# Performance work log

Measured on AMD Instinct MI355X. Metric: run time of the kernel, lower is better.

Reference implementation:

```python
import jax, jax.numpy as jnp
import numpy as np

S, B, E = 512, 512, 768

def setup_inputs() -> dict:
    key = jax.random.key(0)
    k1, k2, k3 = jax.random.split(key, 3)
    inputs = jax.random.normal(k1, (S, B, E), dtype=jnp.float32)
    rotation_params = jax.random.normal(k2, (E, E), dtype=jnp.float32)
    entangle_params = jax.random.normal(k3, (E, E), dtype=jnp.float32)
    return {"inputs": inputs, "rotation_params": rotation_params, "entangle_params": entangle_params}

def reference(inputs, rotation_params, entangle_params):
    seq_len, batch, embed_dim = inputs.shape
    # Q/K projections: (S,B,E) @ (E,E) -> (S,B,E)
    q = jnp.einsum('sbe,ef->sbf', inputs, rotation_params.reshape(embed_dim, -1))
    k = jnp.einsum('sbe,ef->sbf', inputs, entangle_params.reshape(embed_dim, -1))
    v = inputs
    # Faithful to the torch code: matmul batches over seq_len, so attention
    # mixes across the BATCH axis -> scores shape (S, B, B).
    scale = 1.0 / jnp.sqrt(jnp.float32(embed_dim))
    scores = jax.nn.softmax(jnp.einsum('sbe,sce->sbc', q, k) * scale, axis=-1)
    return jnp.einsum('sbc,sce->sbe', scores, v)
```

## Files before the change

kernel.cpp:

```cpp
#include <hip/hip_runtime.h>
#include <hip/hip_bf16.h>
#include <math.h>

typedef unsigned short ushort_t;
typedef __attribute__((ext_vector_type(8))) short bf16x8;
typedef __attribute__((ext_vector_type(4))) float f32x4;

#define SCALE 0.03608439182435161f

__device__ __forceinline__ ushort_t f2bf(float f) {
  unsigned u = __float_as_uint(f);
  return (ushort_t)((u + 0x7FFFu + ((u >> 16) & 1u)) >> 16);
}
__device__ __forceinline__ float bf2f(ushort_t h) {
  return __uint_as_float(((unsigned)h) << 16);
}

__device__ __forceinline__ void split4(float4 v, ushort_t* hh, ushort_t* ll) {
  __hip_bfloat162 h01 = __float22bfloat162_rn(make_float2(v.x, v.y));
  __hip_bfloat162 h23 = __float22bfloat162_rn(make_float2(v.z, v.w));
  unsigned u01 = *(unsigned*)&h01, u23 = *(unsigned*)&h23;
  float l0 = v.x - __uint_as_float((u01 & 0xFFFFu) << 16);
  float l1 = v.y - __uint_as_float(u01 & 0xFFFF0000u);
  float l2 = v.z - __uint_as_float((u23 & 0xFFFFu) << 16);
  float l3 = v.w - __uint_as_float(u23 & 0xFFFF0000u);
  __hip_bfloat162 g01 = __float22bfloat162_rn(make_float2(l0, l1));
  __hip_bfloat162 g23 = __float22bfloat162_rn(make_float2(l2, l3));
  *(unsigned*)&hh[0] = u01; *(unsigned*)&hh[2] = u23;
  *(unsigned*)&ll[0] = *(unsigned*)&g01; *(unsigned*)&ll[2] = *(unsigned*)&g23;
}

struct MMP {
  const float* Af;  long aLd;
  const float* Bf;
  const ushort_t* Bhi; const ushort_t* Blo; long bLd;
  ushort_t* Chi; ushort_t* Clo; long cLd;
  int zMode;
  int K;
};

template <int BM>
__global__ __launch_bounds__(256) void mm(MMP P)
{
  __shared__ ushort_t lds[16384];
  ushort_t* Ah = lds;
  ushort_t* Al = lds + 4096;
  ushort_t* Bh = lds + 8192;
  ushort_t* Bl = lds + 12288;

  const int tid = threadIdx.x;
  int bx = blockIdx.x, by = blockIdx.y;
  {
    int nwg = gridDim.x * gridDim.y;
    if ((nwg & 7) == 0) {
      int id = by * gridDim.x + bx;
      int q = nwg >> 3;
      int wid = (id & 7) * q + (id >> 3);
      bx = wid % gridDim.x;
      by = wid / gridDim.x;
    }
  }
  const int m0 = by * 128, n0 = bx * 128;

  const int lane = tid & 63;
  const int wave = tid >> 6;
  const int wm = (wave >> 1) * 64, wn = (wave & 1) * 64;
  const int lr = lane & 15, g = lane >> 4;

  f32x4 acc[4][4];
  #pragma unroll
  for (int i = 0; i < 4; ++i)
    #pragma unroll
    for (int j = 0; j < 4; ++j) {
      f32x4 zv = {0.f, 0.f, 0.f, 0.f};
      acc[i][j] = zv;
    }

  for (int k0 = 0; k0 < P.K; k0 += 32) {
    #pragma unroll
    for (int rep = 0; rep < 4; ++rep) {
      int idx = tid + rep * 256;
      int row = idx >> 3, q = idx & 7;
      float4 v = *(const float4*)(P.Af + (long)(m0 + row) * P.aLd + k0 + q * 4);
      int off = row * 32 + (((q >> 1) ^ ((row >> 1) & 3)) << 3) + ((q & 1) << 2);
      ushort_t hh[4], ll[4];
      split4(v, hh, ll);
      *(uint2*)(Ah + off) = *(uint2*)hh;
      *(uint2*)(Al + off) = *(uint2*)ll;
    }
    if constexpr (BM == 0) {
      #pragma unroll
      for (int rep = 0; rep < 4; ++rep) {
        int idx = tid + rep * 256;
        int row = idx >> 3, q = idx & 7;
        float4 v = *(const float4*)(P.Bf + (long)(n0 + row) * P.bLd + k0 + q * 4);
        int off = row * 32 + (((q >> 1) ^ ((row >> 1) & 3)) << 3) + ((q & 1) << 2);
        ushort_t hh[4], ll[4];
        split4(v, hh, ll);
        *(uint2*)(Bh + off) = *(uint2*)hh;
        *(uint2*)(Bl + off) = *(uint2*)ll;
      }
    } else {
      #pragma unroll
      for (int rep = 0; rep < 2; ++rep) {
        int idx = tid + rep * 256;
        int row = idx >> 2, h8 = idx & 3;
        int off = row * 32 + ((h8 ^ ((row >> 1) & 3)) << 3);
        long gsrc = (long)(n0 + row) * P.bLd + k0 + h8 * 8;
        *(uint4*)(Bh + off) = *(const uint4*)(P.Bhi + gsrc);
        *(uint4*)(Bl + off) = *(const uint4*)(P.Blo + gsrc);
      }
    }
    __syncthreads();

    bf16x8 ar[4], br[4];
    #pragma unroll
    for (int i = 0; i < 4; ++i) {
      int row = wm + i * 16 + lr;
      ar[i] = *(const bf16x8*)(Ah + row * 32 + ((g ^ ((row >> 1) & 3)) << 3));
    }
    #pragma unroll
    for (int j = 0; j < 4; ++j) {
      int row = wn + j * 16 + lr;
      br[j] = *(const bf16x8*)(Bh + row * 32 + ((g ^ ((row >> 1) & 3)) << 3));
    }
    #pragma unroll
    for (int i = 0; i < 4; ++i)
      #pragma unroll
      for (int j = 0; j < 4; ++j)
        acc[i][j] = __builtin_amdgcn_mfma_f32_16x16x32_bf16(ar[i], br[j], acc[i][j], 0, 0, 0);
    #pragma unroll
    for (int j = 0; j < 4; ++j) {
      int row = wn + j * 16 + lr;
      bf16x8 blv = *(const bf16x8*)(Bl + row * 32 + ((g ^ ((row >> 1) & 3)) << 3));
      #pragma unroll
      for (int i = 0; i < 4; ++i)
        acc[i][j] = __builtin_amdgcn_mfma_f32_16x16x32_bf16(ar[i], blv, acc[i][j], 0, 0, 0);
    }
    #pragma unroll
    for (int i = 0; i < 4; ++i) {
      int row = wm + i * 16 + lr;
      bf16x8 alv = *(const bf16x8*)(Al + row * 32 + ((g ^ ((row >> 1) & 3)) << 3));
      #pragma unroll
      for (int j = 0; j < 4; ++j)
        acc[i][j] = __builtin_amdgcn_mfma_f32_16x16x32_bf16(alv, br[j], acc[i][j], 0, 0, 0);
    }
    __syncthreads();
  }

  #pragma unroll
  for (int i = 0; i < 4; ++i) {
    #pragma unroll
    for (int j = 0; j < 4; ++j) {
      int colG = n0 + wn + j * 16 + lr;
      #pragma unroll
      for (int r = 0; r < 4; ++r) {
        int rowG = m0 + wm + i * 16 + g * 4 + r;
        float v = acc[i][j][r];
        ushort_t hi = f2bf(v);
        ushort_t lo = f2bf(v - bf2f(hi));
        long off;
        if (P.zMode) off = (long)(rowG >> 9) * 786432 + (long)(rowG & 511) * 1536 + colG;
        else         off = (long)rowG * P.cLd + colG;
        P.Chi[off] = hi;
        P.Clo[off] = lo;
      }
    }
  }
}

__global__ __launch_bounds__(512) void fsc5(ushort_t* __restrict__ slots,
                                            const float* __restrict__ X)
{
  __shared__ ushort_t lds[36864];
  ushort_t* Ah = lds;
  ushort_t* Al = lds + 2048;
  ushort_t* Bh = lds + 4096;
  ushort_t* Bl = lds + 20480;
  float* redf = (float*)lds;
  float* reds = (float*)lds + 768;

  const int id = blockIdx.x;
  const int c = id & 7, r = id >> 3;
  const int tile = r & 7;
  const int s = c + ((r >> 3) << 3);
  const int m0 = tile * 64;

  ushort_t* Az = slots + (long)s * 786432;
  const float* Xf = X + (long)s * 393216;

  const int tid = threadIdx.x;
  const int lane = tid & 63;
  const int wave = tid >> 6;
  const int wn = wave * 64;
  const int lr = lane & 15, g = lane >> 4;

  f32x4 acc[4][4];
  #pragma unroll
  for (int i = 0; i < 4; ++i)
    #pragma unroll
    for (int j = 0; j < 4; ++j) {
      f32x4 zv = {0.f, 0.f, 0.f, 0.f};
      acc[i][j] = zv;
    }

  for (int k0 = 0; k0 < 768; k0 += 32) {
    {
      int e = tid & 255;
      int row = e >> 2, h8 = e & 3;
      int off = row * 32 + ((h8 ^ ((row >> 1) & 3)) << 3);
      long src = (long)(m0 + row) * 1536 + k0 + h8 * 8;
      if (tid < 256) *(uint4*)(Ah + off) = *(const uint4*)(Az + src);
      else           *(uint4*)(Al + off) = *(const uint4*)(Az + src + 768);
    }
    #pragma unroll
    for (int rep = 0; rep < 8; ++rep) {
      int idx = tid + rep * 512;
      int row = idx >> 3, q = idx & 7;
      float4 v = *(const float4*)(Xf + (long)row * 768 + k0 + q * 4);
      int off = row * 32 + (((q >> 1) ^ ((row >> 1) & 3)) << 3) + ((q & 1) << 2);
      ushort_t hh[4], ll[4];
      split4(v, hh, ll);
      *(uint2*)(Bh + off) = *(uint2*)hh;
      *(uint2*)(Bl + off) = *(uint2*)ll;
    }
    __syncthreads();

    bf16x8 arh[4], arl[4];
    #pragma unroll
    for (int i = 0; i < 4; ++i) {
      int row = i * 16 + lr;
      int off = row * 32 + ((g ^ ((row >> 1) & 3)) << 3);
      arh[i] = *(const bf16x8*)(Ah + off);
      arl[i] = *(const bf16x8*)(Al + off);
    }
    #pragma unroll
    for (int j = 0; j < 4; ++j) {
      int row = wn + j * 16 + lr;
      int off = row * 32 + ((g ^ ((row >> 1) & 3)) << 3);
      bf16x8 bh = *(const bf16x8*)(Bh + off);
      bf16x8 bl = *(const bf16x8*)(Bl + off);
      #pragma unroll
      for (int i = 0; i < 4; ++i) {
        acc[i][j] = __builtin_amdgcn_mfma_f32_16x16x32_bf16(arh[i], bh, acc[i][j], 0, 0, 0);
        acc[i][j] = __builtin_amdgcn_mfma_f32_16x16x32_bf16(arh[i], bl, acc[i][j], 0, 0, 0);
        acc[i][j] = __builtin_amdgcn_mfma_f32_16x16x32_bf16(arl[i], bh, acc[i][j], 0, 0, 0);
      }
    }
    __syncthreads();
  }

  float mr[4][4];
  #pragma unroll
  for (int i = 0; i < 4; ++i)
    #pragma unroll
    for (int rg = 0; rg < 4; ++rg) {
      float mx = -3.0e38f;
      #pragma unroll
      for (int j = 0; j < 4; ++j) {
        acc[i][j][rg] *= SCALE;
        mx = fmaxf(mx, acc[i][j][rg]);
      }
      #pragma unroll
      for (int off = 8; off >= 1; off >>= 1) mx = fmaxf(mx, __shfl_xor(mx, off, 64));
      if (lr == 0) redf[(i * 16 + g * 4 + rg) * 12 + wave] = mx;
    }
  __syncthreads();
  #pragma unroll
  for (int i = 0; i < 4; ++i)
    #pragma unroll
    for (int rg = 0; rg < 4; ++rg) {
      int row = i * 16 + g * 4 + rg;
      float4 a = *(const float4*)&redf[row * 12];
      float4 b = *(const float4*)&redf[row * 12 + 4];
      mr[i][rg] = fmaxf(fmaxf(fmaxf(a.x, a.y), fmaxf(a.z, a.w)),
                        fmaxf(fmaxf(b.x, b.y), fmaxf(b.z, b.w)));
    }
  #pragma unroll
  for (int i = 0; i < 4; ++i)
    #pragma unroll
    for (int rg = 0; rg < 4; ++rg) {
      float sm = 0.f;
      #pragma unroll
      for (int j = 0; j < 4; ++j) {
        float e = __expf(acc[i][j][rg] - mr[i][rg]);
        acc[i][j][rg] = e;
        sm += e;
      }
      #pragma unroll
      for (int off = 8; off >= 1; off >>= 1) sm += __shfl_xor(sm, off, 64);
      if (lr == 0) reds[(i * 16 + g * 4 + rg) * 12 + wave] = sm;
    }
  __syncthreads();
  #pragma unroll
  for (int i = 0; i < 4; ++i)
    #pragma unroll
    for (int rg = 0; rg < 4; ++rg) {
      int row = i * 16 + g * 4 + rg;
      float4 a = *(const float4*)&reds[row * 12];
      float4 b = *(const float4*)&reds[row * 12 + 4];
      float inv = 1.0f / (a.x + a.y + a.z + a.w + b.x + b.y + b.z + b.w);
      #pragma unroll
      for (int j = 0; j < 4; ++j)
        Az[(long)(m0 + row) * 1536 + wn + j * 16 + lr] = f2bf(acc[i][j][rg] * inv);
    }
}

__global__ __launch_bounds__(768) void pv(float* __restrict__ outp,
                                          const float* __restrict__ X)
{
  __shared__ ushort_t Pa[32768];

  const int id = blockIdx.x;
  const int c = id & 7, r = id >> 3;
  const int tile = r & 7;
  const int s = c + ((r >> 3) << 3);
  const int m0 = tile * 64;

  const ushort_t* Ps = (const ushort_t*)outp + (long)s * 786432;
  const float* Xf = X + (long)s * 393216;

  const int tid = threadIdx.x;
  const int lane = tid & 63;
  const int wave = tid >> 6;
  const int wn = wave * 64;
  const int lr = lane & 15, g = lane >> 4;

  for (int idx = tid; idx < 4096; idx += 768) {
    int row = idx >> 6, h8 = idx & 63;
    int off = row * 512 + ((h8 ^ (row & 7)) << 3);
    *(uint4*)(Pa + off) = *(const uint4*)(Ps + (long)(m0 + row) * 1536 + h8 * 8);
  }
  __syncthreads();

  f32x4 acc[4][4];
  #pragma unroll
  for (int i = 0; i < 4; ++i)
    #pragma unroll
    for (int j = 0; j < 4; ++j) {
      f32x4 zv = {0.f, 0.f, 0.f, 0.f};
      acc[i][j] = zv;
    }

  for (int kk = 0; kk < 16; ++kk) {
    const int k0 = kk * 32;
    bf16x8 ar[4];
    #pragma unroll
    for (int i = 0; i < 4; ++i) {
      int row = i * 16 + lr;
      ar[i] = *(const bf16x8*)(Pa + row * 512 + (((kk * 4 + g) ^ (row & 7)) << 3));
    }
    #pragma unroll
    for (int j = 0; j < 4; ++j) {
      int col = wn + j * 16 + lr;
      float xv[8];
      #pragma unroll
      for (int i = 0; i < 8; ++i)
        xv[i] = Xf[(long)(k0 + g * 8 + i) * 768 + col];
      unsigned w[4];
      #pragma unroll
      for (int p = 0; p < 4; ++p) {
        __hip_bfloat162 hb = __float22bfloat162_rn(make_float2(xv[2 * p], xv[2 * p + 1]));
        w[p] = *(unsigned*)&hb;
      }
      bf16x8 bv = *(bf16x8*)w;
      #pragma unroll
      for (int i = 0; i < 4; ++i)
        acc[i][j] = __builtin_amdgcn_mfma_f32_16x16x32_bf16(ar[i], bv, acc[i][j], 0, 0, 0);
    }
  }

  float* Co = outp + (long)s * 393216;
  #pragma unroll
  for (int i = 0; i < 4; ++i)
    #pragma unroll
    for (int j = 0; j < 4; ++j) {
      int colG = wn + j * 16 + lr;
      #pragma unroll
      for (int rg = 0; rg < 4; ++rg) {
        int rowG = m0 + i * 16 + g * 4 + rg;
        Co[(long)rowG * 768 + colG] = acc[i][j][rg];
      }
    }
}

extern "C" void kernel_launch(void* const* d_in, const int* in_sizes, int n_in,
                              void* d_out, int out_size, void* d_ws, size_t ws_size,
                              hipStream_t stream) {
  const float* X = (const float*)d_in[0];
  const float* R = (const float*)d_in[1];
  const float* W = (const float*)d_in[2];

  ushort_t* Hhi = (ushort_t*)d_ws;
  ushort_t* Hlo = Hhi + 768 * 768;

  {
    MMP p{};
    p.Af = W; p.aLd = 768;
    p.Bf = R; p.bLd = 768;
    p.Chi = Hhi; p.Clo = Hlo; p.cLd = 768; p.zMode = 0;
    p.K = 768;
    mm<0><<<dim3(6, 6), 256, 0, stream>>>(p);
  }
  {
    MMP p{};
    p.Af = X; p.aLd = 768;
    p.Bhi = Hhi; p.Blo = Hlo; p.bLd = 768;
    p.Chi = (ushort_t*)d_out;
    p.Clo = (ushort_t*)d_out + 768;
    p.zMode = 1;
    p.K = 768;
    mm<1><<<dim3(6, 2048), 256, 0, stream>>>(p);
  }
  fsc5<<<dim3(4096), 512, 0, stream>>>((ushort_t*)d_out, X);
  pv<<<dim3(4096), 768, 0, stream>>>((float*)d_out, X);
}
```

Baseline: 3.074 ms.

## Double-buffer LDS tiles in score kernel with register prefetch of next K slice

The score kernel now keeps two LDS buffers. It prefetches the next K slice of A and X into registers while MFMAs run on the current buffer, then writes the prefetch into the other buffer, so each step needs one barrier instead of two. The MFMA loop is also reordered into three independent passes over all 16 accumulators so that dependent MFMAs are spaced further apart. The cost is twice the LDS footprint (144KB) and many more live registers, and a launch_bounds hint of 2 blocks per CU that the LDS size may not allow.

After: 3.113 ms. Within noise of the previous version (+1.2%).

```diff
diff --git a/kernel.cpp b/kernel.cpp
--- a/kernel.cpp
+++ b/kernel.cpp
@@ -169,14 +169,10 @@
   }
 }
 
-__global__ __launch_bounds__(512) void fsc5(ushort_t* __restrict__ slots,
-                                            const float* __restrict__ X)
+__global__ __launch_bounds__(512, 2) void fsc6(ushort_t* __restrict__ slots,
+                                               const float* __restrict__ X)
 {
-  __shared__ ushort_t lds[36864];
-  ushort_t* Ah = lds;
-  ushort_t* Al = lds + 2048;
-  ushort_t* Bh = lds + 4096;
-  ushort_t* Bl = lds + 20480;
+  __shared__ ushort_t lds[73728];
   float* redf = (float*)lds;
   float* reds = (float*)lds + 768;
 
@@ -195,6 +191,12 @@
   const int wn = wave * 64;
   const int lr = lane & 15, g = lane >> 4;
 
+  const int ae = tid & 255;
+  const int arow = ae >> 2, ah8 = ae & 3;
+  const int aoff = arow * 32 + ((ah8 ^ ((arow >> 1) & 3)) << 3);
+  const long asrc = (long)(m0 + arow) * 1536 + ah8 * 8 + (tid < 256 ? 0 : 768);
+  const int adst = aoff + (tid < 256 ? 0 : 2048);
+
   f32x4 acc[4][4];
   #pragma unroll
   for (int i = 0; i < 4; ++i)
@@ -204,49 +206,90 @@
       acc[i][j] = zv;
     }
 
-  for (int k0 = 0; k0 < 768; k0 += 32) {
-    {
-      int e = tid & 255;
-      int row = e >> 2, h8 = e & 3;
-      int off = row * 32 + ((h8 ^ ((row >> 1) & 3)) << 3);
-      long src = (long)(m0 + row) * 1536 + k0 + h8 * 8;
-      if (tid < 256) *(uint4*)(Ah + off) = *(const uint4*)(Az + src);
-      else           *(uint4*)(Al + off) = *(const uint4*)(Az + src + 768);
-    }
-    #pragma unroll
-    for (int rep = 0; rep < 8; ++rep) {
-      int idx = tid + rep * 512;
-      int row = idx >> 3, q = idx & 7;
-      float4 v = *(const float4*)(Xf + (long)row * 768 + k0 + q * 4);
-      int off = row * 32 + (((q >> 1) ^ ((row >> 1) & 3)) << 3) + ((q & 1) << 2);
-      ushort_t hh[4], ll[4];
-      split4(v, hh, ll);
-      *(uint2*)(Bh + off) = *(uint2*)hh;
-      *(uint2*)(Bl + off) = *(uint2*)ll;
-    }
-    __syncthreads();
-
-    bf16x8 arh[4], arl[4];
+  float4 bv0, bv1, bv2, bv3, bv4, bv5, bv6, bv7;
+  uint4 av;
+
+#define FSC_LOAD(K0)                                                         \
+  do {                                                                       \
+    av = *(const uint4*)(Az + asrc + (K0));                                  \
+    const float* xb = Xf + (K0);                                             \
+    bv0 = *(const float4*)(xb + (long)((tid + 0 * 512) >> 3) * 768 + ((tid + 0 * 512) & 7) * 4); \
+    bv1 = *(const float4*)(xb + (long)((tid + 1 * 512) >> 3) * 768 + ((tid + 1 * 512) & 7) * 4); \
+    bv2 = *(const float4*)(xb + (long)((tid + 2 * 512) >> 3) * 768 + ((tid + 2 * 512) & 7) * 4); \
+    bv3 = *(const float4*)(xb + (long)((tid + 3 * 512) >> 3) * 768 + ((tid + 3 * 512) & 7) * 4); \
+    bv4 = *(const float4*)(xb + (long)((tid + 4 * 512) >> 3) * 768 + ((tid + 4 * 512) & 7) * 4); \
+    bv5 = *(const float4*)(xb + (long)((tid + 5 * 512) >> 3) * 768 + ((tid + 5 * 512) & 7) * 4); \
+    bv6 = *(const float4*)(xb + (long)((tid + 6 * 512) >> 3) * 768 + ((tid + 6 * 512) & 7) * 4); \
+    bv7 = *(const float4*)(xb + (long)((tid + 7 * 512) >> 3) * 768 + ((tid + 7 * 512) & 7) * 4); \
+  } while (0)
+
+#define FSC_WR1(BH, BL, BV, REP)                                             \
+  do {                                                                       \
+    int idx = tid + (REP) * 512;                                             \
+    int row = idx >> 3, q = idx & 7;                                         \
+    int off = row * 32 + (((q >> 1) ^ ((row >> 1) & 3)) << 3) + ((q & 1) << 2); \
+    ushort_t hh[4], ll[4];                                                   \
+    split4(BV, hh, ll);                                                      \
+    *(uint2*)((BH) + off) = *(uint2*)hh;                                     \
+    *(uint2*)((BL) + off) = *(uint2*)ll;                                     \
+  } while (0)
+
+#define FSC_WRITE(B)                                                         \
+  do {                                                                       \
+    ushort_t* Ab = lds + (B) * 4096;                                         \
+    ushort_t* Bhw = lds + 8192 + (B) * 32768;                                \
+    ushort_t* Blw = Bhw + 16384;                                             \
+    *(uint4*)(Ab + adst) = av;                                               \
+    FSC_WR1(Bhw, Blw, bv0, 0); FSC_WR1(Bhw, Blw, bv1, 1);                    \
+    FSC_WR1(Bhw, Blw, bv2, 2); FSC_WR1(Bhw, Blw, bv3, 3);                    \
+    FSC_WR1(Bhw, Blw, bv4, 4); FSC_WR1(Bhw, Blw, bv5, 5);                    \
+    FSC_WR1(Bhw, Blw, bv6, 6); FSC_WR1(Bhw, Blw, bv7, 7);                    \
+  } while (0)
+
+  FSC_LOAD(0);
+  FSC_WRITE(0);
+  __syncthreads();
+
+  for (int t = 0; t < 24; ++t) {
+    const int cb = t & 1;
+    if (t < 23) FSC_LOAD((t + 1) * 32);
+
+    const ushort_t* Ab = lds + cb * 4096;
+    const ushort_t* Bh = lds + 8192 + cb * 32768;
+    const ushort_t* Bl = Bh + 16384;
+
+    bf16x8 arh[4], arl[4], bh[4], bl[4];
     #pragma unroll
     for (int i = 0; i < 4; ++i) {
       int row = i * 16 + lr;
       int off = row * 32 + ((g ^ ((row >> 1) & 3)) << 3);
-      arh[i] = *(const bf16x8*)(Ah + off);
-      arl[i] = *(const bf16x8*)(Al + off);
+      arh[i] = *(const bf16x8*)(Ab + off);
+      arl[i] = *(const bf16x8*)(Ab + 2048 + off);
     }
     #pragma unroll
     for (int j = 0; j < 4; ++j) {
       int row = wn + j * 16 + lr;
       int off = row * 32 + ((g ^ ((row >> 1) & 3)) << 3);
-      bf16x8 bh = *(const bf16x8*)(Bh + off);
-      bf16x8 bl = *(const bf16x8*)(Bl + off);
-      #pragma unroll
-      for (int i = 0; i < 4; ++i) {
-        acc[i][j] = __builtin_amdgcn_mfma_f32_16x16x32_bf16(arh[i], bh, acc[i][j], 0, 0, 0);
-        acc[i][j] = __builtin_amdgcn_mfma_f32_16x16x32_bf16(arh[i], bl, acc[i][j], 0, 0, 0);
-        acc[i][j] = __builtin_amdgcn_mfma_f32_16x16x32_bf16(arl[i], bh, acc[i][j], 0, 0, 0);
-      }
-    }
+      bh[j] = *(const bf16x8*)(Bh + off);
+      bl[j] = *(const bf16x8*)(Bl + off);
+    }
+    #pragma unroll
+    for (int i = 0; i < 4; ++i)
+      #pragma unroll
+      for (int j = 0; j < 4; ++j)
+        acc[i][j] = __builtin_amdgcn_mfma_f32_16x16x32_bf16(arh[i], bh[j], acc[i][j], 0, 0, 0);
+    #pragma unroll
+    for (int i = 0; i < 4; ++i)
+      #pragma unroll
+      for (int j = 0; j < 4; ++j)
+        acc[i][j] = __builtin_amdgcn_mfma_f32_16x16x32_bf16(arh[i], bl[j], acc[i][j], 0, 0, 0);
+    #pragma unroll
+    for (int i = 0; i < 4; ++i)
+      #pragma unroll
+      for (int j = 0; j < 4; ++j)
+        acc[i][j] = __builtin_amdgcn_mfma_f32_16x16x32_bf16(arl[i], bh[j], acc[i][j], 0, 0, 0);
+
+    if (t < 23) FSC_WRITE(1 - cb);
     __syncthreads();
   }
 
@@ -412,6 +455,6 @@
     p.K = 768;
     mm<1><<<dim3(6, 2048), 256, 0, stream>>>(p);
   }
-  fsc5<<<dim3(4096), 512, 0, stream>>>((ushort_t*)d_out, X);
+  fsc6<<<dim3(4096), 512, 0, stream>>>((ushort_t*)d_out, X);
   pv<<<dim3(4096), 768, 0, stream>>>((float*)d_out, X);
 }
```
